# Kernel optimization log

Measured on AMD Instinct MI355X. Metric: run time of the kernel, lower is better.

Reference implementation:

```python
import jax, jax.numpy as jnp
import numpy as np

N = 4096        # num_of_drugs / nodes
EMB = 256       # emb_size
ATT = 128       # atten_size
H = 3           # nheads
PAIRS = 131072  # scored drug pairs
ALPHA = 0.2     # LeakyReLU slope in GraphAttentionLayer
NEG = -9e15     # pyGAT mask value


def setup_inputs() -> dict:
    key = jax.random.key(0)
    ks = jax.random.split(key, 14)
    s = 0.05
    return dict(
        a_idx=jax.random.randint(ks[0], (PAIRS,), 0, N),
        b_idx=jax.random.randint(ks[1], (PAIRS,), 0, N),
        adj=jax.random.randint(ks[2], (N, N), 0, 2).astype(jnp.int32),
        emb=jax.random.normal(ks[3], (N, EMB)) * s,          # nn.Embedding table
        emb_b=jax.random.normal(ks[4], (N, 1)) * s,          # bias embedding table
        W1=jax.random.normal(ks[5], (H, EMB, ATT)) * s,      # layer-1 head weights
        av1=jax.random.normal(ks[6], (H, 2 * ATT, 1)) * s,   # layer-1 attn vectors
        W2=jax.random.normal(ks[7], (H, H * ATT, ATT)) * s,  # layer-2 head weights
        av2=jax.random.normal(ks[8], (H, 2 * ATT, 1)) * s,   # layer-2 attn vectors
        a_mix=jax.random.normal(ks[9], (1, 1)),              # self.a
        b_mix=jax.random.normal(ks[10], (1, 1)),             # self.b
        lin_W=jax.random.normal(ks[11], (H * ATT, ATT)) * s,
        lin_b=jnp.zeros((ATT,)),
        out_W=jax.random.normal(ks[12], (ATT + 1, 1)) * s,
        out_b=jnp.zeros((1,)),
    )


def _gat_head(h, W, av, mask):
    # standard pyGAT dense GraphAttentionLayer (eval mode, concat=True)
    Wh = h @ W                                   # [N, F]
    f = Wh.shape[1]
    e = jax.nn.leaky_relu(Wh @ av[:f] + (Wh @ av[f:]).T, ALPHA)  # [N, N]
    e = jnp.where(mask, e, NEG)
    att = jax.nn.softmax(e, axis=1)
    return jax.nn.elu(att @ Wh)                  # [N, F]


def _gat_multi(h, Ws, avs, mask):
    outs = jax.vmap(lambda W, av: _gat_head(h, W, av, mask))(Ws, avs)  # [H, N, F]
    Hn, Nn, Fn = outs.shape
    return jnp.transpose(outs, (1, 0, 2)).reshape(Nn, Hn * Fn)  # cat over heads, dim=1


def reference(a_idx, b_idx, adj, emb, emb_b, W1, av1, W2, av2,
              a_mix, b_mix, lin_W, lin_b, out_W, out_b):
    mask = adj > 0
    at1 = _gat_multi(emb, W1, av1, mask)   # [N, H*ATT]
    at2 = _gat_multi(at1, W2, av2, mask)   # [N, H*ATT]
    denom = a_mix + b_mix
    atten = at1 * (a_mix / denom) + at2 * (b_mix / denom)
    x = atten[a_idx] * atten[b_idx]        # index_select + elementwise mul
    x = jax.nn.gelu(x @ lin_W + lin_b, approximate=False)
    b_add = jax.nn.gelu(emb_b[a_idx] + emb_b[b_idx], approximate=False)
    x = jnp.concatenate([x, b_add], axis=1)
    return jax.nn.sigmoid(x @ out_W + out_b)  # [PAIRS, 1]
```

## Files before the change

### kernel.cpp

```cpp
#include <hip/hip_runtime.h>

typedef unsigned long long u64;
typedef unsigned short u16;
typedef __bf16 bf16_t;
typedef bf16_t bf16x8 __attribute__((ext_vector_type(8)));
typedef float f32x4 __attribute__((ext_vector_type(4)));
typedef float f32x2 __attribute__((ext_vector_type(2)));

#define NN 4096
#define NH 3
#define NPAIR 131072
#define LOG2E 1.4426950408889634f

#if __has_builtin(__builtin_amdgcn_cvt_pk_fp8_f32) && \
    __has_builtin(__builtin_amdgcn_cvt_pk_f32_fp8)
#define HAVE_FP8_CVT 1
#else
#define HAVE_FP8_CVT 0
#endif

union U8 { uint4 u; bf16x8 b; };

__device__ __forceinline__ u16 f2us(float f) {
  unsigned int x = __float_as_uint(f);
  x = x + 0x7fffu + ((x >> 16) & 1u);
  return (u16)(x >> 16);
}
__device__ __forceinline__ float us2f(u16 u) {
  return __uint_as_float(((unsigned int)u) << 16);
}
__device__ __forceinline__ unsigned int pk2(float a, float b) {
  return (unsigned int)f2us(a) | ((unsigned int)f2us(b) << 16);
}
__device__ __forceinline__ float geluf(float x) {
  return 0.5f * x * (1.f + erff(x * 0.70710678118654752f));
}
__device__ __forceinline__ float exp2fast(float x) {
#if __has_builtin(__builtin_amdgcn_exp2f)
  return __builtin_amdgcn_exp2f(x);
#else
  return __expf(x * 0.6931471805599453f);
#endif
}
__device__ __forceinline__ void gl_lds16(const u16* g, u16* s) {
  __builtin_amdgcn_global_load_lds(
      (const __attribute__((address_space(1))) unsigned int*)g,
      (__attribute__((address_space(3))) unsigned int*)s, 16, 0, 0);
}

#if !HAVE_FP8_CVT
__device__ __forceinline__ float e4m3_f(unsigned int b) {
  unsigned int s = b >> 7, e = (b >> 3) & 15, m = b & 7;
  float v = (e == 0) ? (float)m * 0.001953125f
                     : __uint_as_float(((e + 120u) << 23) | (m << 20));
  return s ? -v : v;
}
__device__ __forceinline__ unsigned int f_e4m3(float f) {
  unsigned int sign = (__float_as_uint(f) >> 24) & 0x80u;
  float a = fabsf(f);
  if (!(a >= 9.765625e-4f)) return sign;
  a = fminf(a, 448.f);
  int e;
  float fr = frexpf(a, &e);
  if (e >= -5) {
    int M = (int)(fr * 16.f + 0.5f);
    int E = e + 6;
    if (M == 16) { M = 8; E += 1; }
    if (E > 15) { E = 15; M = 15; }
    return sign | (unsigned)(E << 3) | (unsigned)(M - 8);
  }
  int M = (int)(a * 512.f + 0.5f);
  if (M > 7) M = 7;
  return sign | (unsigned)M;
}
#endif

__device__ __forceinline__ void dec8lo(uint4 u, float* o) {
#if HAVE_FP8_CVT
  f32x2 p0 = __builtin_amdgcn_cvt_pk_f32_fp8((int)u.x, false);
  f32x2 p1 = __builtin_amdgcn_cvt_pk_f32_fp8((int)u.x, true);
  f32x2 p2 = __builtin_amdgcn_cvt_pk_f32_fp8((int)u.y, false);
  f32x2 p3 = __builtin_amdgcn_cvt_pk_f32_fp8((int)u.y, true);
  o[0] = p0[0]; o[1] = p0[1]; o[2] = p1[0]; o[3] = p1[1];
  o[4] = p2[0]; o[5] = p2[1]; o[6] = p3[0]; o[7] = p3[1];
#else
#pragma unroll
  for (int e = 0; e < 4; ++e) o[e] = e4m3_f((u.x >> (8 * e)) & 0xffu);
#pragma unroll
  for (int e = 0; e < 4; ++e) o[4 + e] = e4m3_f((u.y >> (8 * e)) & 0xffu);
#endif
}
__device__ __forceinline__ void dec8hi(uint4 u, float* o) {
#if HAVE_FP8_CVT
  f32x2 p0 = __builtin_amdgcn_cvt_pk_f32_fp8((int)u.z, false);
  f32x2 p1 = __builtin_amdgcn_cvt_pk_f32_fp8((int)u.z, true);
  f32x2 p2 = __builtin_amdgcn_cvt_pk_f32_fp8((int)u.w, false);
  f32x2 p3 = __builtin_amdgcn_cvt_pk_f32_fp8((int)u.w, true);
  o[0] = p0[0]; o[1] = p0[1]; o[2] = p1[0]; o[3] = p1[1];
  o[4] = p2[0]; o[5] = p2[1]; o[6] = p3[0]; o[7] = p3[1];
#else
#pragma unroll
  for (int e = 0; e < 4; ++e) o[e] = e4m3_f((u.z >> (8 * e)) & 0xffu);
#pragma unroll
  for (int e = 0; e < 4; ++e) o[4 + e] = e4m3_f((u.w >> (8 * e)) & 0xffu);
#endif
}

__global__ __launch_bounds__(256) void k_bitmask(const int* __restrict__ adj,
                                                 u64* __restrict__ bm) {
  int i = blockIdx.x;
  int lane = threadIdx.x & 63;
  int wv = threadIdx.x >> 6;
  const int* row = adj + (size_t)i * NN;
  for (int wq = wv; wq < NN / 64; wq += 4) {
    u64 b = __ballot(row[wq * 64 + lane] > 0);
    if (lane == 0) bm[(size_t)i * (NN / 64) + wq] = b;
  }
}

__global__ __launch_bounds__(256) void k_maskf(const u64* __restrict__ bm,
                                               unsigned int* __restrict__ bmF) {
  int idx = blockIdx.x * 256 + threadIdx.x;
  int l = idx & 63, jc = (idx >> 6) & 127, ib = idx >> 13;
  int li = l & 15, lg = l >> 4;
  const unsigned char* b8 = (const unsigned char*)bm;
  unsigned int v = 0;
#pragma unroll
  for (int m = 0; m < 4; ++m)
    v |= (unsigned int)b8[(size_t)(ib * 64 + m * 16 + li) * 512 + jc * 4 + lg]
         << (8 * m);
  bmF[idx] = v;
}

__global__ __launch_bounds__(256) void k_prep(
    const float* __restrict__ emb, const float* __restrict__ W1,
    const float* __restrict__ W2, const float* __restrict__ linW,
    u16* __restrict__ emb16, u16* __restrict__ WT1, u16* __restrict__ WT2,
    u16* __restrict__ linWT) {
  int idx = blockIdx.x * 256 + threadIdx.x;
  if (idx < 1048576) { emb16[idx] = f2us(emb[idx]); return; }
  idx -= 1048576;
  if (idx < 98304) {
    int h = idx / 32768, r = idx & 32767, f = r >> 8, k = r & 255;
    WT1[idx] = f2us(W1[h * 32768 + k * 128 + f]);
    return;
  }
  idx -= 98304;
  if (idx < 147456) {
    int h = idx / 49152, r = idx % 49152, f = r / 384, k = r % 384;
    WT2[idx] = f2us(W2[h * 49152 + k * 128 + f]);
    return;
  }
  idx -= 147456;
  if (idx < 49152) {
    int f = idx / 384, k = idx % 384;
    linWT[idx] = f2us(linW[k * 128 + f]);
  }
}

template <int K>
__global__ __launch_bounds__(64, 4) void k_wh(const u16* __restrict__ xb,
                                              const u16* __restrict__ WT,
                                              const float* __restrict__ av,
                                              u16* __restrict__ WhTF,
                                              float* __restrict__ E1,
                                              float* __restrict__ F1,
                                              float* __restrict__ E2,
                                              float* __restrict__ F2) {
  constexpr int NS = K / 32;
  int h = blockIdx.y, l = threadIdx.x, li = l & 15, lg = l >> 4;
  int iw = blockIdx.x * 16;
  const u16* Wb = WT + (size_t)h * 128 * K;
  const u16* xr = xb + (size_t)(iw + li) * K;

  f32x4 acc[8];
#pragma unroll
  for (int nt = 0; nt < 8; ++nt) acc[nt] = (f32x4){0.f, 0.f, 0.f, 0.f};

#pragma unroll 2
  for (int s = 0; s < NS; ++s) {
    int j0 = s * 32 + lg * 8;
    uint4 xa = *(const uint4*)(xr + j0);
    uint4 b[8];
#pragma unroll
    for (int nt = 0; nt < 8; ++nt)
      b[nt] = *(const uint4*)(Wb + (size_t)(nt * 16 + li) * K + j0);
    U8 af;
    af.u = xa;
#pragma unroll
    for (int nt = 0; nt < 8; ++nt) {
      U8 bb;
      bb.u = b[nt];
      acc[nt] = __builtin_amdgcn_mfma_f32_16x16x32_bf16(af.b, bb.b, acc[nt], 0, 0, 0);
    }
  }

  float p1[4] = {0.f, 0.f, 0.f, 0.f}, p2[4] = {0.f, 0.f, 0.f, 0.f};
#pragma unroll
  for (int nt = 0; nt < 8; ++nt) {
    float a1 = av[h * 256 + nt * 16 + li];
    float a2 = av[h * 256 + 128 + nt * 16 + li];
#pragma unroll
    for (int r = 0; r < 4; ++r) {
      p1[r] = fmaf(acc[nt][r], a1, p1[r]);
      p2[r] = fmaf(acc[nt][r], a2, p2[r]);
    }
  }
#pragma unroll
  for (int r = 0; r < 4; ++r) {
#pragma unroll
    for (int o = 1; o < 16; o <<= 1) {
      p1[r] += __shfl_xor(p1[r], o);
      p2[r] += __shfl_xor(p2[r], o);
    }
  }
  if (li == 0) {
#pragma unroll
    for (int r = 0; r < 4; ++r) {
      int idx = h * NN + iw + lg * 4 + r;
      float s1L = p1[r] * LOG2E, s2L = p2[r] * LOG2E;
      E1[idx] = exp2fast(s1L);
      F1[idx] = exp2fast(0.2f * s1L);
      E2[idx] = exp2fast(s2L);
      F2[idx] = exp2fast(0.2f * s2L);
    }
  }
  u16* Wo = WhTF + (size_t)h * 524288;
  int jc = iw >> 5, jin = (iw & 31) + lg * 4;
#pragma unroll
  for (int nt = 0; nt < 8; ++nt) {
    uint2 pw;
    pw.x = pk2(acc[nt][0], acc[nt][1]);
    pw.y = pk2(acc[nt][2], acc[nt][3]);
    *(uint2*)(Wo + (size_t)nt * 65536 + (size_t)jc * 512 + li * 32 + jin) = pw;
  }
}

#define WAITC(N)                                                  \
  do {                                                            \
    asm volatile("s_waitcnt vmcnt(" #N ")" ::: "memory");         \
    __builtin_amdgcn_sched_barrier(0);                            \
    __builtin_amdgcn_s_barrier();                                 \
    __builtin_amdgcn_sched_barrier(0);                            \
  } while (0)
#define ROT3(X) X = (X == 2) ? 0 : X + 1

__global__ __launch_bounds__(256, 3) void k_acc(
    const unsigned int* __restrict__ bmF, const u16* __restrict__ WhTF,
    const float* __restrict__ E1, const float* __restrict__ F1,
    const float* __restrict__ E2, const float* __restrict__ F2,
    u16* __restrict__ Pp, float* __restrict__ dnP) {
  __shared__ __align__(16) u16 Bl[3][4096];
  int h = blockIdx.y, t = threadIdx.x, w = t >> 6, l = t & 63;
  int li = l & 15, lg = l >> 4;
  int rt = blockIdx.x >> 3, kq = blockIdx.x & 7;
  int iw0 = rt * 128 + w * 32;
  int k0 = kq * 512;
  int perm = (l & 15) * 4 + (l >> 4);
  const u16* gsrcA = WhTF + (size_t)h * 524288 + (size_t)w * 65536 +
                     (size_t)(k0 >> 5) * 512 + perm * 8;
  const u16* gsrcB = gsrcA + (size_t)4 * 65536;
  const float* E2h = E2 + h * NN;
  const float* F2h = F2 + h * NN;
  float e1v[2], f1v[2];
  e1v[0] = E1[h * NN + iw0 + li];
  e1v[1] = E1[h * NN + iw0 + 16 + li];
  f1v[0] = F1[h * NN + iw0 + li];
  f1v[1] = F1[h * NN + iw0 + 16 + li];
  int mq0 = (iw0 >> 4) & 3;
  const unsigned int* mrow =
      bmF + ((size_t)(iw0 >> 6) * 128 + (k0 >> 5)) * 64 + l;

  f32x4 acc[2][8];
  f32x4 accD[2];
#pragma unroll
  for (int mg = 0; mg < 2; ++mg) {
    accD[mg] = (f32x4){0.f, 0.f, 0.f, 0.f};
#pragma unroll
    for (int nt = 0; nt < 8; ++nt) acc[mg][nt] = (f32x4){0.f, 0.f, 0.f, 0.f};
  }
  U8 ones;
  ones.u = make_uint4(0x3F803F80u, 0x3F803F80u, 0x3F803F80u, 0x3F803F80u);

#define STG2(B, S)                                        \
  do {                                                    \
    gl_lds16(gsrcA + (size_t)(S) * 512, &Bl[B][w * 512]); \
    gl_lds16(gsrcB + (size_t)(S) * 512, &Bl[B][(w + 4) * 512]); \
  } while (0)
#define LDSC(SUF, S)                                      \
  do {                                                    \
    int j0_ = k0 + (S) * 32;                              \
    mw##SUF = mrow[(S) * 64];                             \
    e2a##SUF = *(const float4*)(E2h + j0_ + lg * 8);      \
    e2b##SUF = *(const float4*)(E2h + j0_ + lg * 8 + 4);  \
    f2a##SUF = *(const float4*)(F2h + j0_ + lg * 8);      \
    f2b##SUF = *(const float4*)(F2h + j0_ + lg * 8 + 4);  \
  } while (0)
#define BODY(SUF)                                                            \
  do {                                                                       \
    float ea_[8] = {e2a##SUF.x, e2a##SUF.y, e2a##SUF.z, e2a##SUF.w,          \
                    e2b##SUF.x, e2b##SUF.y, e2b##SUF.z, e2b##SUF.w};         \
    float fa_[8] = {f2a##SUF.x, f2a##SUF.y, f2a##SUF.z, f2a##SUF.w,          \
                    f2b##SUF.x, f2b##SUF.y, f2b##SUF.z, f2b##SUF.w};         \
    U8 A_[2];                                                                \
    _Pragma("unroll") for (int mg = 0; mg < 2; ++mg) {                       \
      unsigned int mb_ = (mw##SUF >> (8 * (mq0 + mg))) & 0xffu;              \
      _Pragma("unroll") for (int e = 0; e < 8; ++e) {                        \
        float v_ = fmaxf(e1v[mg] * ea_[e], f1v[mg] * fa_[e]);                \
        A_[mg].b[e] = (bf16_t)(((mb_ >> e) & 1u) ? v_ : 0.f);                \
      }                                                                      \
    }                                                                        \
    const u16* bl_ = &Bl[bcur][0] + l * 8;                                   \
    _Pragma("unroll") for (int nt = 0; nt < 8; ++nt) {                       \
      U8 B_;                                                                 \
      B_.u = *(const uint4*)(bl_ + nt * 512);                                \
      acc[0][nt] = __builtin_amdgcn_mfma_f32_16x16x32_bf16(A_[0].b, B_.b,    \
                                                  acc[0][nt], 0, 0, 0);      \
      acc[1][nt] = __builtin_amdgcn_mfma_f32_16x16x32_bf16(A_[1].b, B_.b,    \
                                                  acc[1][nt], 0, 0, 0);      \
    }                                                                        \
    accD[0] = __builtin_amdgcn_mfma_f32_16x16x32_bf16(A_[0].b, ones.b,       \
                                                      accD[0], 0, 0, 0);     \
    accD[1] = __builtin_amdgcn_mfma_f32_16x16x32_bf16(A_[1].b, ones.b,       \
                                                      accD[1], 0, 0, 0);     \
    ROT3(bcur);                                                              \
  } while (0)

  unsigned int mwA, mwB;
  float4 e2aA, e2bA, f2aA, f2bA, e2aB, e2bB, f2aB, f2bB;
  int bcur = 0, bstg = 2;
  LDSC(A, 0);
  STG2(0, 0);
  STG2(1, 1);
#pragma unroll 1
  for (int s = 0; s < 16; s += 2) {
    WAITC(2);
    LDSC(B, s + 1);
    if (s + 2 < 16) { STG2(bstg, s + 2); ROT3(bstg); }
    BODY(A);
    if (s + 1 == 15) { WAITC(0); } else { WAITC(2); }
    if (s + 2 < 16) LDSC(A, s + 2);
    if (s + 3 < 16) { STG2(bstg, s + 3); ROT3(bstg); }
    BODY(B);
  }
#undef STG2
#undef LDSC
#undef BODY

#pragma unroll
  for (int mg = 0; mg < 2; ++mg) {
    size_t rbase = (size_t)(kq * 3 + h) * NN + iw0 + mg * 16;
#pragma unroll
    for (int nt = 0; nt < 8; ++nt)
#pragma unroll
      for (int r = 0; r < 4; ++r)
        Pp[(rbase + lg * 4 + r) * 128 + nt * 16 + li] = f2us(acc[mg][nt][r]);
    if (li == 0) {
#pragma unroll
      for (int r = 0; r < 4; ++r)
        dnP[rbase + lg * 4 + r] = accD[mg][r];
    }
  }
}

__global__ __launch_bounds__(256) void k_fin(
    const u16* __restrict__ Pp, const float* __restrict__ dnP,
    const float* __restrict__ at1f_in, const float* __restrict__ amix,
    const float* __restrict__ bmix, float* __restrict__ at1f_out,
    u16* __restrict__ at1b_out, unsigned char* __restrict__ att8_out,
    int mode) {
  int gid = blockIdx.x * 256 + threadIdx.x;
  int c4 = gid & 31, row = (gid >> 5) & 4095, h = gid >> 17;
  size_t off = ((size_t)h * NN + row) * 128 + c4 * 4;
  const size_t ks = (size_t)3 * NN * 128;
  float s[4] = {0.f, 0.f, 0.f, 0.f};
  float dsum = 0.f;
#pragma unroll
  for (int q = 0; q < 8; ++q) {
    uint2 v = *(const uint2*)(Pp + q * ks + off);
    s[0] += us2f((u16)(v.x & 0xffffu));
    s[1] += us2f((u16)(v.x >> 16));
    s[2] += us2f((u16)(v.y & 0xffffu));
    s[3] += us2f((u16)(v.y >> 16));
    dsum += dnP[(size_t)(q * 3 + h) * NN + row];
  }
  float inv = 1.f / fmaxf(dsum, 1e-30f);
#pragma unroll
  for (int q = 0; q < 4; ++q) {
    s[q] *= inv;
    s[q] = s[q] > 0.f ? s[q] : (exp2fast(s[q] * LOG2E) - 1.f);
  }
  size_t oi = (size_t)row * 384 + h * 128 + c4 * 4;
  if (mode == 0) {
    *(float4*)(at1f_out + oi) = make_float4(s[0], s[1], s[2], s[3]);
    uint2 pb;
    pb.x = pk2(s[0], s[1]);
    pb.y = pk2(s[2], s[3]);
    *(uint2*)(at1b_out + oi) = pb;
  } else {
    float Am = amix[0], Bm = bmix[0];
    float wa = Am / (Am + Bm), wb = Bm / (Am + Bm);
    float4 a1 = *(const float4*)(at1f_in + oi);
    float m0 = wa * a1.x + wb * s[0];
    float m1 = wa * a1.y + wb * s[1];
    float m2 = wa * a1.z + wb * s[2];
    float m3 = wa * a1.w + wb * s[3];
#if HAVE_FP8_CVT
    int v8 = __builtin_amdgcn_cvt_pk_fp8_f32(m0, m1, 0, false);
    v8 = __builtin_amdgcn_cvt_pk_fp8_f32(m2, m3, v8, true);
#else
    unsigned int v8 = f_e4m3(m0) | (f_e4m3(m1) << 8) | (f_e4m3(m2) << 16) |
                      (f_e4m3(m3) << 24);
#endif
    int gc = h * 128 + c4 * 4;
    int st = gc >> 5, lg2 = (gc >> 3) & 3, e0 = gc & 7;
    int kp = (st >> 1) * 64 + lg2 * 16 + (st & 1) * 8 + e0;
    *(unsigned int*)(att8_out + (size_t)row * 384 + kp) = (unsigned int)v8;
  }
}

__global__ __launch_bounds__(1024) void k_pairs(
    const int* __restrict__ aidx, const int* __restrict__ bidx,
    const unsigned char* __restrict__ att8, const u16* __restrict__ linWT,
    const float* __restrict__ linB, const float* __restrict__ outW,
    const float* __restrict__ outB, const float* __restrict__ embB,
    float* __restrict__ out) {
  __shared__ __align__(16) u16 Wlds[128][392];
  int t = threadIdx.x, w = t >> 6, l = t & 63;
  int li = l & 15, lg = l >> 4;
  {
    int r = t >> 3, seg = (t & 7) * 48;
    const u16* src = linWT + (size_t)r * 384 + seg;
    u16* dst = &Wlds[r][seg];
#pragma unroll
    for (int q = 0; q < 6; ++q)
      *(uint4*)(dst + q * 8) = *(const uint4*)(src + q * 8);
  }
  __syncthreads();

  int p0 = blockIdx.x * 512 + w * 32;
  int ia0 = aidx[p0 + li], ib0 = bidx[p0 + li];
  int ia1 = aidx[p0 + 16 + li], ib1 = bidx[p0 + 16 + li];
  const unsigned char* ra0 = att8 + (size_t)ia0 * 384;
  const unsigned char* rb0 = att8 + (size_t)ib0 * 384;
  const unsigned char* ra1 = att8 + (size_t)ia1 * 384;
  const unsigned char* rb1 = att8 + (size_t)ib1 * 384;
  int boff = lg * 16;

  f32x4 acc[2][8];
#pragma unroll
  for (int g = 0; g < 2; ++g)
#pragma unroll
    for (int nt = 0; nt < 8; ++nt) acc[g][nt] = (f32x4){0.f, 0.f, 0.f, 0.f};

#define LDG8(BUF, S2)                               \
  do {                                              \
    int o_ = (S2) * 64 + boff;                      \
    BUF[0] = *(const uint4*)(ra0 + o_);             \
    BUF[1] = *(const uint4*)(rb0 + o_);             \
    BUF[2] = *(const uint4*)(ra1 + o_);             \
    BUF[3] = *(const uint4*)(rb1 + o_);             \
  } while (0)
#define WORK8(BUF, S2)                                                       \
  do {                                                                       \
    _Pragma("unroll") for (int hf = 0; hf < 2; ++hf) {                       \
      float a0_[8], b0_[8], a1_[8], b1_[8];                                  \
      if (hf == 0) {                                                         \
        dec8lo(BUF[0], a0_); dec8lo(BUF[1], b0_);                            \
        dec8lo(BUF[2], a1_); dec8lo(BUF[3], b1_);                            \
      } else {                                                               \
        dec8hi(BUF[0], a0_); dec8hi(BUF[1], b0_);                            \
        dec8hi(BUF[2], a1_); dec8hi(BUF[3], b1_);                            \
      }                                                                      \
      U8 af0_, af1_;                                                         \
      _Pragma("unroll") for (int e = 0; e < 8; ++e) {                        \
        af0_.b[e] = (bf16_t)(a0_[e] * b0_[e]);                               \
        af1_.b[e] = (bf16_t)(a1_[e] * b1_[e]);                               \
      }                                                                      \
      int j0_ = ((S2) * 2 + hf) * 32 + lg * 8;                               \
      _Pragma("unroll") for (int nt = 0; nt < 8; ++nt) {                     \
        U8 bb_;                                                              \
        bb_.u = *(const uint4*)&Wlds[nt * 16 + li][j0_];                     \
        acc[0][nt] = __builtin_amdgcn_mfma_f32_16x16x32_bf16(af0_.b, bb_.b,  \
                                                    acc[0][nt], 0, 0, 0);    \
        acc[1][nt] = __builtin_amdgcn_mfma_f32_16x16x32_bf16(af1_.b, bb_.b,  \
                                                    acc[1][nt], 0, 0, 0);    \
      }                                                                      \
    }                                                                        \
  } while (0)

  uint4 bX[4], bY[4], bZ[4];
  LDG8(bX, 0);
  LDG8(bY, 1);
  LDG8(bZ, 2);
  WORK8(bX, 0);
  LDG8(bX, 3);
  WORK8(bY, 1);
  LDG8(bY, 4);
  WORK8(bZ, 2);
  LDG8(bZ, 5);
  WORK8(bX, 3);
  WORK8(bY, 4);
  WORK8(bZ, 5);
#undef LDG8
#undef WORK8

#pragma unroll
  for (int g = 0; g < 2; ++g) {
    float z[4] = {0.f, 0.f, 0.f, 0.f};
#pragma unroll
    for (int nt = 0; nt < 8; ++nt) {
      int f = nt * 16 + li;
      float lb = linB[f], ow = outW[f];
#pragma unroll
      for (int r = 0; r < 4; ++r) {
        float y = geluf(acc[g][nt][r] + lb);
        z[r] = fmaf(y, ow, z[r]);
      }
    }
#pragma unroll
    for (int r = 0; r < 4; ++r) {
      z[r] += __shfl_xor(z[r], 1);
      z[r] += __shfl_xor(z[r], 2);
      z[r] += __shfl_xor(z[r], 4);
      z[r] += __shfl_xor(z[r], 8);
    }
    if (li == 0) {
#pragma unroll
      for (int r = 0; r < 4; ++r) {
        int pi = p0 + g * 16 + lg * 4 + r;
        float badd = geluf(embB[aidx[pi]] + embB[bidx[pi]]);
        float zz = z[r] + badd * outW[128] + outB[0];
        out[pi] = 1.f / (1.f + __expf(-zz));
      }
    }
  }
}

extern "C" void kernel_launch(void* const* d_in, const int* in_sizes, int n_in,
                              void* d_out, int out_size, void* d_ws, size_t ws_size,
                              hipStream_t stream) {
  (void)in_sizes; (void)n_in; (void)out_size; (void)ws_size;
  const int* aidx = (const int*)d_in[0];
  const int* bidx = (const int*)d_in[1];
  const int* adj = (const int*)d_in[2];
  const float* emb = (const float*)d_in[3];
  const float* embB = (const float*)d_in[4];
  const float* W1 = (const float*)d_in[5];
  const float* av1 = (const float*)d_in[6];
  const float* W2 = (const float*)d_in[7];
  const float* av2 = (const float*)d_in[8];
  const float* amix = (const float*)d_in[9];
  const float* bmix = (const float*)d_in[10];
  const float* linW = (const float*)d_in[11];
  const float* linB = (const float*)d_in[12];
  const float* outW = (const float*)d_in[13];
  const float* outB = (const float*)d_in[14];

  char* ws = (char*)d_ws;
  u64* bm = (u64*)(ws + 0);
  u16* WhTF = (u16*)(ws + (2u << 20));
  float* E1 = (float*)(ws + (5u << 20));
  float* F1 = (float*)(ws + (5u << 20) + (64u << 10));
  float* E2 = (float*)(ws + (5u << 20) + (128u << 10));
  float* F2 = (float*)(ws + (5u << 20) + (192u << 10));
  u16* linWT = (u16*)(ws + (5u << 20) + (256u << 10));
  u16* WT1 = (u16*)(ws + (5u << 20) + (384u << 10));
  u16* WT2 = (u16*)(ws + (5u << 20) + (640u << 10));
  float* at1f = (float*)(ws + (6u << 20));
  u16* sh12 = (u16*)(ws + (12u << 20));
  u16* emb16 = sh12;
  u16* at1b = sh12;
  unsigned int* bmF = (unsigned int*)(ws + (15u << 20));
  u16* Pp = (u16*)(ws + (17u << 20));
  float* dnP = (float*)(ws + (41u << 20));
  unsigned char* att8 = (unsigned char*)(ws + (42u << 20));

  k_bitmask<<<NN, 256, 0, stream>>>(adj, bm);
  k_maskf<<<2048, 256, 0, stream>>>(bm, bmF);
  k_prep<<<5248, 256, 0, stream>>>(emb, W1, W2, linW, emb16, WT1, WT2, linWT);
  k_wh<256><<<dim3(256, NH), 64, 0, stream>>>(emb16, WT1, av1, WhTF, E1, F1, E2, F2);
  k_acc<<<dim3(256, NH), 256, 0, stream>>>(bmF, WhTF, E1, F1, E2, F2, Pp, dnP);
  k_fin<<<1536, 256, 0, stream>>>(Pp, dnP, at1f, amix, bmix, at1f, at1b, att8, 0);
  k_wh<384><<<dim3(256, NH), 64, 0, stream>>>(at1b, WT2, av2, WhTF, E1, F1, E2, F2);
  k_acc<<<dim3(256, NH), 256, 0, stream>>>(bmF, WhTF, E1, F1, E2, F2, Pp, dnP);
  k_fin<<<1536, 256, 0, stream>>>(Pp, dnP, at1f, amix, bmix, at1f, at1b, att8, 1);
  k_pairs<<<NPAIR / 512, 1024, 0, stream>>>(aidx, bidx, att8, linWT, linB, outW,
                                            outB, embB, (float*)d_out);
}
```

Baseline: 164.0 us.

## Sort pairs by a_idx via counting sort to improve gather locality

Adds histogram, scan and scatter kernels that build a permutation of pairs sorted by the first drug index. The pair-scoring kernel then processes pairs in sorted order, reading indices through the permutation and writing outputs to the original positions. The aim is better cache reuse of the fp8 attention rows gathered per pair. It adds three kernel launches, a memset, atomics, and scattered output writes.

```diff
diff --git a/kernel.cpp b/kernel.cpp
--- a/kernel.cpp
+++ b/kernel.cpp
@@ -156,6 +156,46 @@
     int f = idx / 384, k = idx % 384;
     linWT[idx] = f2us(linW[k * 128 + f]);
   }
+}
+
+__global__ __launch_bounds__(256) void k_hist(const int* __restrict__ aidx,
+                                              unsigned int* __restrict__ hist) {
+  int p = blockIdx.x * 256 + threadIdx.x;
+  atomicAdd(&hist[aidx[p]], 1u);
+}
+
+__global__ __launch_bounds__(256) void k_scan(
+    const unsigned int* __restrict__ hist, unsigned int* __restrict__ cursor) {
+  int t = threadIdx.x, l = t & 63, w = t >> 6;
+  unsigned int v[16], s = 0;
+#pragma unroll
+  for (int q = 0; q < 16; ++q) {
+    v[q] = s;
+    s += hist[t * 16 + q];
+  }
+  unsigned int inc = s;
+#pragma unroll
+  for (int o = 1; o < 64; o <<= 1) {
+    unsigned int u = __shfl_up(inc, o, 64);
+    if (l >= o) inc += u;
+  }
+  unsigned int wave_excl = inc - s;
+  __shared__ unsigned int wsum[4];
+  if (l == 63) wsum[w] = inc;
+  __syncthreads();
+  unsigned int wbase = 0;
+  for (int ww = 0; ww < w; ++ww) wbase += wsum[ww];
+  unsigned int base = wbase + wave_excl;
+#pragma unroll
+  for (int q = 0; q < 16; ++q) cursor[t * 16 + q] = base + v[q];
+}
+
+__global__ __launch_bounds__(256) void k_scatter(
+    const int* __restrict__ aidx, unsigned int* __restrict__ cursor,
+    int* __restrict__ perm) {
+  int p = blockIdx.x * 256 + threadIdx.x;
+  unsigned int pos = atomicAdd(&cursor[aidx[p]], 1u);
+  perm[pos] = p;
 }
 
 template <int K>
@@ -421,10 +461,10 @@
 
 __global__ __launch_bounds__(1024) void k_pairs(
     const int* __restrict__ aidx, const int* __restrict__ bidx,
-    const unsigned char* __restrict__ att8, const u16* __restrict__ linWT,
-    const float* __restrict__ linB, const float* __restrict__ outW,
-    const float* __restrict__ outB, const float* __restrict__ embB,
-    float* __restrict__ out) {
+    const int* __restrict__ perm, const unsigned char* __restrict__ att8,
+    const u16* __restrict__ linWT, const float* __restrict__ linB,
+    const float* __restrict__ outW, const float* __restrict__ outB,
+    const float* __restrict__ embB, float* __restrict__ out) {
   __shared__ __align__(16) u16 Wlds[128][392];
   int t = threadIdx.x, w = t >> 6, l = t & 63;
   int li = l & 15, lg = l >> 4;
@@ -439,8 +479,9 @@
   __syncthreads();
 
   int p0 = blockIdx.x * 512 + w * 32;
-  int ia0 = aidx[p0 + li], ib0 = bidx[p0 + li];
-  int ia1 = aidx[p0 + 16 + li], ib1 = bidx[p0 + 16 + li];
+  int sp0 = perm[p0 + li], sp1 = perm[p0 + 16 + li];
+  int ia0 = aidx[sp0], ib0 = bidx[sp0];
+  int ia1 = aidx[sp1], ib1 = bidx[sp1];
   const unsigned char* ra0 = att8 + (size_t)ia0 * 384;
   const unsigned char* rb0 = att8 + (size_t)ib0 * 384;
   const unsigned char* ra1 = att8 + (size_t)ia1 * 384;
@@ -528,10 +569,10 @@
     if (li == 0) {
 #pragma unroll
       for (int r = 0; r < 4; ++r) {
-        int pi = p0 + g * 16 + lg * 4 + r;
-        float badd = geluf(embB[aidx[pi]] + embB[bidx[pi]]);
+        int sp = perm[p0 + g * 16 + lg * 4 + r];
+        float badd = geluf(embB[aidx[sp]] + embB[bidx[sp]]);
         float zz = z[r] + badd * outW[128] + outB[0];
-        out[pi] = 1.f / (1.f + __expf(-zz));
+        out[sp] = 1.f / (1.f + __expf(-zz));
       }
     }
   }
@@ -575,7 +616,14 @@
   u16* Pp = (u16*)(ws + (17u << 20));
   float* dnP = (float*)(ws + (41u << 20));
   unsigned char* att8 = (unsigned char*)(ws + (42u << 20));
-
+  unsigned int* hist = (unsigned int*)(ws + (43u << 20) + (512u << 10));
+  unsigned int* cursor = (unsigned int*)(ws + (43u << 20) + (528u << 10));
+  int* perm = (int*)(ws + (43u << 20) + (544u << 10));
+
+  hipMemsetAsync(hist, 0, 4096 * sizeof(unsigned int), stream);
+  k_hist<<<NPAIR / 256, 256, 0, stream>>>(aidx, hist);
+  k_scan<<<1, 256, 0, stream>>>(hist, cursor);
+  k_scatter<<<NPAIR / 256, 256, 0, stream>>>(aidx, cursor, perm);
   k_bitmask<<<NN, 256, 0, stream>>>(adj, bm);
   k_maskf<<<2048, 256, 0, stream>>>(bm, bmF);
   k_prep<<<5248, 256, 0, stream>>>(emb, W1, W2, linW, emb16, WT1, WT2, linWT);
@@ -585,6 +633,6 @@
   k_wh<384><<<dim3(256, NH), 64, 0, stream>>>(at1b, WT2, av2, WhTF, E1, F1, E2, F2);
   k_acc<<<dim3(256, NH), 256, 0, stream>>>(bmF, WhTF, E1, F1, E2, F2, Pp, dnP);
   k_fin<<<1536, 256, 0, stream>>>(Pp, dnP, at1f, amix, bmix, at1f, at1b, att8, 1);
-  k_pairs<<<NPAIR / 512, 1024, 0, stream>>>(aidx, bidx, att8, linWT, linB, outW,
-                                            outB, embB, (float*)d_out);
-}
+  k_pairs<<<NPAIR / 512, 1024, 0, stream>>>(aidx, bidx, perm, att8, linWT, linB,
+                                            outW, outB, embB, (float*)d_out);
+}
```

Measured after the change: 195.5 us. +19.2%, slower.

## Give each k_acc wave 64 rows with 128-thread blocks

Applied to the files above, without the earlier changes.

The attention-times-Wh accumulation kernel now launches 2 waves of 128 threads per block instead of 4 waves of 256 threads. Each wave covers 64 rows (4 MFMA row groups) rather than 32. Each LDS B-fragment load is therefore reused across 4 MFMAs instead of 2, and each wave stages 4 slices per step. The cost is roughly double the accumulator registers (launch bounds lowered to 2) and half the waves per block, which reduces occupancy and latency hiding.

```diff
diff --git a/kernel.cpp b/kernel.cpp
--- a/kernel.cpp
+++ b/kernel.cpp
@@ -245,7 +245,7 @@
   } while (0)
 #define ROT3(X) X = (X == 2) ? 0 : X + 1
 
-__global__ __launch_bounds__(256, 3) void k_acc(
+__global__ __launch_bounds__(128, 2) void k_acc(
     const unsigned int* __restrict__ bmF, const u16* __restrict__ WhTF,
     const float* __restrict__ E1, const float* __restrict__ F1,
     const float* __restrict__ E2, const float* __restrict__ F2,
@@ -254,27 +254,29 @@
   int h = blockIdx.y, t = threadIdx.x, w = t >> 6, l = t & 63;
   int li = l & 15, lg = l >> 4;
   int rt = blockIdx.x >> 3, kq = blockIdx.x & 7;
-  int iw0 = rt * 128 + w * 32;
+  int iw0 = rt * 128 + w * 64;
   int k0 = kq * 512;
   int perm = (l & 15) * 4 + (l >> 4);
-  const u16* gsrcA = WhTF + (size_t)h * 524288 + (size_t)w * 65536 +
+  const u16* gsrc0 = WhTF + (size_t)h * 524288 + (size_t)(w * 4) * 65536 +
                      (size_t)(k0 >> 5) * 512 + perm * 8;
-  const u16* gsrcB = gsrcA + (size_t)4 * 65536;
+  const u16* gsrc1 = gsrc0 + (size_t)65536;
+  const u16* gsrc2 = gsrc0 + (size_t)2 * 65536;
+  const u16* gsrc3 = gsrc0 + (size_t)3 * 65536;
   const float* E2h = E2 + h * NN;
   const float* F2h = F2 + h * NN;
-  float e1v[2], f1v[2];
-  e1v[0] = E1[h * NN + iw0 + li];
-  e1v[1] = E1[h * NN + iw0 + 16 + li];
-  f1v[0] = F1[h * NN + iw0 + li];
-  f1v[1] = F1[h * NN + iw0 + 16 + li];
-  int mq0 = (iw0 >> 4) & 3;
+  float e1v[4], f1v[4];
+#pragma unroll
+  for (int mg = 0; mg < 4; ++mg) {
+    e1v[mg] = E1[h * NN + iw0 + mg * 16 + li];
+    f1v[mg] = F1[h * NN + iw0 + mg * 16 + li];
+  }
   const unsigned int* mrow =
       bmF + ((size_t)(iw0 >> 6) * 128 + (k0 >> 5)) * 64 + l;
 
-  f32x4 acc[2][8];
-  f32x4 accD[2];
-#pragma unroll
-  for (int mg = 0; mg < 2; ++mg) {
+  f32x4 acc[4][8];
+  f32x4 accD[4];
+#pragma unroll
+  for (int mg = 0; mg < 4; ++mg) {
     accD[mg] = (f32x4){0.f, 0.f, 0.f, 0.f};
 #pragma unroll
     for (int nt = 0; nt < 8; ++nt) acc[mg][nt] = (f32x4){0.f, 0.f, 0.f, 0.f};
@@ -282,10 +284,12 @@
   U8 ones;
   ones.u = make_uint4(0x3F803F80u, 0x3F803F80u, 0x3F803F80u, 0x3F803F80u);
 
-#define STG2(B, S)                                        \
-  do {                                                    \
-    gl_lds16(gsrcA + (size_t)(S) * 512, &Bl[B][w * 512]); \
-    gl_lds16(gsrcB + (size_t)(S) * 512, &Bl[B][(w + 4) * 512]); \
+#define STG4(B, S)                                                \
+  do {                                                            \
+    gl_lds16(gsrc0 + (size_t)(S) * 512, &Bl[B][(w * 4 + 0) * 512]); \
+    gl_lds16(gsrc1 + (size_t)(S) * 512, &Bl[B][(w * 4 + 1) * 512]); \
+    gl_lds16(gsrc2 + (size_t)(S) * 512, &Bl[B][(w * 4 + 2) * 512]); \
+    gl_lds16(gsrc3 + (size_t)(S) * 512, &Bl[B][(w * 4 + 3) * 512]); \
   } while (0)
 #define LDSC(SUF, S)                                      \
   do {                                                    \
@@ -302,9 +306,9 @@
                     e2b##SUF.x, e2b##SUF.y, e2b##SUF.z, e2b##SUF.w};         \
     float fa_[8] = {f2a##SUF.x, f2a##SUF.y, f2a##SUF.z, f2a##SUF.w,          \
                     f2b##SUF.x, f2b##SUF.y, f2b##SUF.z, f2b##SUF.w};         \
-    U8 A_[2];                                                                \
-    _Pragma("unroll") for (int mg = 0; mg < 2; ++mg) {                       \
-      unsigned int mb_ = (mw##SUF >> (8 * (mq0 + mg))) & 0xffu;              \
+    U8 A_[4];                                                                \
+    _Pragma("unroll") for (int mg = 0; mg < 4; ++mg) {                       \
+      unsigned int mb_ = (mw##SUF >> (8 * mg)) & 0xffu;                      \
       _Pragma("unroll") for (int e = 0; e < 8; ++e) {                        \
         float v_ = fmaxf(e1v[mg] * ea_[e], f1v[mg] * fa_[e]);                \
         A_[mg].b[e] = (bf16_t)(((mb_ >> e) & 1u) ? v_ : 0.f);                \
@@ -318,11 +322,14 @@
                                                   acc[0][nt], 0, 0, 0);      \
       acc[1][nt] = __builtin_amdgcn_mfma_f32_16x16x32_bf16(A_[1].b, B_.b,    \
                                                   acc[1][nt], 0, 0, 0);      \
+      acc[2][nt] = __builtin_amdgcn_mfma_f32_16x16x32_bf16(A_[2].b, B_.b,    \
+                                                  acc[2][nt], 0, 0, 0);      \
+      acc[3][nt] = __builtin_amdgcn_mfma_f32_16x16x32_bf16(A_[3].b, B_.b,    \
+                                                  acc[3][nt], 0, 0, 0);      \
     }                                                                        \
-    accD[0] = __builtin_amdgcn_mfma_f32_16x16x32_bf16(A_[0].b, ones.b,       \
-                                                      accD[0], 0, 0, 0);     \
-    accD[1] = __builtin_amdgcn_mfma_f32_16x16x32_bf16(A_[1].b, ones.b,       \
-                                                      accD[1], 0, 0, 0);     \
+    _Pragma("unroll") for (int mg = 0; mg < 4; ++mg)                         \
+      accD[mg] = __builtin_amdgcn_mfma_f32_16x16x32_bf16(A_[mg].b, ones.b,   \
+                                                   accD[mg], 0, 0, 0);       \
     ROT3(bcur);                                                              \
   } while (0)
 
@@ -330,25 +337,25 @@
   float4 e2aA, e2bA, f2aA, f2bA, e2aB, e2bB, f2aB, f2bB;
   int bcur = 0, bstg = 2;
   LDSC(A, 0);
-  STG2(0, 0);
-  STG2(1, 1);
+  STG4(0, 0);
+  STG4(1, 1);
 #pragma unroll 1
   for (int s = 0; s < 16; s += 2) {
-    WAITC(2);
+    WAITC(4);
     LDSC(B, s + 1);
-    if (s + 2 < 16) { STG2(bstg, s + 2); ROT3(bstg); }
+    if (s + 2 < 16) { STG4(bstg, s + 2); ROT3(bstg); }
     BODY(A);
-    if (s + 1 == 15) { WAITC(0); } else { WAITC(2); }
+    if (s + 1 == 15) { WAITC(0); } else { WAITC(4); }
     if (s + 2 < 16) LDSC(A, s + 2);
-    if (s + 3 < 16) { STG2(bstg, s + 3); ROT3(bstg); }
+    if (s + 3 < 16) { STG4(bstg, s + 3); ROT3(bstg); }
     BODY(B);
   }
-#undef STG2
+#undef STG4
 #undef LDSC
 #undef BODY
 
 #pragma unroll
-  for (int mg = 0; mg < 2; ++mg) {
+  for (int mg = 0; mg < 4; ++mg) {
     size_t rbase = (size_t)(kq * 3 + h) * NN + iw0 + mg * 16;
 #pragma unroll
     for (int nt = 0; nt < 8; ++nt)
@@ -580,10 +587,10 @@
   k_maskf<<<2048, 256, 0, stream>>>(bm, bmF);
   k_prep<<<5248, 256, 0, stream>>>(emb, W1, W2, linW, emb16, WT1, WT2, linWT);
   k_wh<256><<<dim3(256, NH), 64, 0, stream>>>(emb16, WT1, av1, WhTF, E1, F1, E2, F2);
-  k_acc<<<dim3(256, NH), 256, 0, stream>>>(bmF, WhTF, E1, F1, E2, F2, Pp, dnP);
+  k_acc<<<dim3(256, NH), 128, 0, stream>>>(bmF, WhTF, E1, F1, E2, F2, Pp, dnP);
   k_fin<<<1536, 256, 0, stream>>>(Pp, dnP, at1f, amix, bmix, at1f, at1b, att8, 0);
   k_wh<384><<<dim3(256, NH), 64, 0, stream>>>(at1b, WT2, av2, WhTF, E1, F1, E2, F2);
-  k_acc<<<dim3(256, NH), 256, 0, stream>>>(bmF, WhTF, E1, F1, E2, F2, Pp, dnP);
+  k_acc<<<dim3(256, NH), 128, 0, stream>>>(bmF, WhTF, E1, F1, E2, F2, Pp, dnP);
   k_fin<<<1536, 256, 0, stream>>>(Pp, dnP, at1f, amix, bmix, at1f, at1b, att8, 1);
   k_pairs<<<NPAIR / 512, 1024, 0, stream>>>(aidx, bidx, att8, linWT, linB, outW,
                                             outB, embB, (float*)d_out);
```

After: 174.5 us. +6.4%, slower.
